# Optimization experiments

Hardware: AMD Instinct MI355X
Metric: run time of the kernel (lower is better)

Reference implementation:

```python
import jax, jax.numpy as jnp
import numpy as np

N_NODES = 50000
N_EDGES = 600000
CHANNELS = 128
HEADS = 8


def setup_inputs() -> dict:
    key = jax.random.key(0)
    k1, k2, k3 = jax.random.split(key, 3)
    x = jax.random.normal(k1, (N_NODES, CHANNELS), dtype=jnp.float32)
    edge_index = jax.random.randint(k2, (2, N_EDGES), 0, N_NODES, dtype=jnp.int32)
    att = jax.random.normal(k3, (HEADS, 2 * (CHANNELS // HEADS)), dtype=jnp.float32)
    return {"x": x, "edge_index": edge_index, "att": att}


def reference(x, edge_index, att):
    # x: [N, C], edge_index: [2, E], att: [H, 2*D] with D = C // H
    src, dst = edge_index[0], edge_index[1]
    n = x.shape[0]
    h = att.shape[0]
    d = att.shape[1] // 2

    x_src = x[src].reshape(-1, h, d)   # [E, H, D]
    x_dst = x[dst].reshape(-1, h, d)   # [E, H, D]

    # (cat([x_src, x_dst]) * att).sum(-1) == x_src @ att[:, :D] + x_dst @ att[:, D:]
    a_src, a_dst = att[:, :d], att[:, d:]
    alpha = jnp.einsum('ehd,hd->eh', x_src, a_src) + jnp.einsum('ehd,hd->eh', x_dst, a_dst)
    alpha = jnp.where(alpha >= 0, alpha, 0.2 * alpha)  # LeakyReLU(0.2)

    # segment softmax over dst; torch scatter_reduce amax includes the zero init,
    # so the per-node max is max(segment_max, 0)
    seg_max = jax.ops.segment_max(alpha, dst, num_segments=n)  # [N, H]
    seg_max = jnp.maximum(seg_max, 0.0)
    alpha = jnp.exp(alpha - seg_max[dst])
    seg_sum = jax.ops.segment_sum(alpha, dst, num_segments=n)  # [N, H]
    alpha = alpha / jnp.maximum(seg_sum[dst], 1e-10)

    # weighted scatter-add of source features
    weighted = x_src * alpha[..., None]                        # [E, H, D]
    out = jax.ops.segment_sum(weighted, dst, num_segments=n)   # [N, H, D]
    return out.reshape(n, -1)
```

## Files before the change

### kernel.cpp

```cpp
#include <hip/hip_runtime.h>

#define N_NODES  50000
#define N_EDGES  600000
#define CHANNELS 128
#define HEADS    8
#define HEAD_DIM 16
#define CAP      64

#define NBINS    256
#define CHUNK_E  1024
#define NCHUNK   ((N_EDGES + CHUNK_E - 1) / CHUNK_E)
#define SEGCAP   2816
#define NPB      200

#define LOGIT_VB ((N_NODES * (CHANNELS / 4)) / 256)
#define WPB      4

__global__ void hist_logit_kernel(const float* __restrict__ x,
                                  const float* __restrict__ att,
                                  const int*   __restrict__ dst,
                                  int*            __restrict__ hist,
                                  float*          __restrict__ ls8,
                                  float*          __restrict__ ld8,
                                  unsigned short* __restrict__ xb) {
    int b = blockIdx.x;
    int t = threadIdx.x;
    if (b < NCHUNK) {
        __shared__ int lh[NBINS];
        lh[t] = 0;
        __syncthreads();
        int base = b * CHUNK_E;
#pragma unroll
        for (int k = 0; k < 4; ++k) {
            int e = base + t + k * 256;
            if (e < N_EDGES) {
                unsigned bin = (unsigned)(dst[e] * NBINS) / N_NODES;
                atomicAdd(&lh[bin], 1);
            }
        }
        __syncthreads();
        hist[t * NCHUNK + b] = lh[t];
    } else {
        int gid = (b - NCHUNK) * 256 + t;
        int n  = gid >> 5;
        int c4 = gid & 31;
        int h  = c4 >> 2;
        int j4 = c4 & 3;

        float4 v = ((const float4*)x)[gid];

        unsigned int ux = __float_as_uint(v.x), uy = __float_as_uint(v.y);
        unsigned int uz = __float_as_uint(v.z), uw = __float_as_uint(v.w);
        ushort4 pk;
        pk.x = (unsigned short)((ux + 0x7FFFu + ((ux >> 16) & 1u)) >> 16);
        pk.y = (unsigned short)((uy + 0x7FFFu + ((uy >> 16) & 1u)) >> 16);
        pk.z = (unsigned short)((uz + 0x7FFFu + ((uz >> 16) & 1u)) >> 16);
        pk.w = (unsigned short)((uw + 0x7FFFu + ((uw >> 16) & 1u)) >> 16);
        ((ushort4*)xb)[gid] = pk;

        float4 as4 = ((const float4*)att)[h * 8 + j4];
        float4 ad4 = ((const float4*)att)[h * 8 + 4 + j4];
        float ts = v.x * as4.x + v.y * as4.y + v.z * as4.z + v.w * as4.w;
        float td = v.x * ad4.x + v.y * ad4.y + v.z * ad4.z + v.w * ad4.w;
        ts += __shfl_xor(ts, 1, 4); ts += __shfl_xor(ts, 2, 4);
        td += __shfl_xor(td, 1, 4); td += __shfl_xor(td, 2, 4);
        if (j4 == 0) {
            ls8[n * HEADS + h] = ts;
            ld8[n * HEADS + h] = td;
        }
    }
}

__global__ void scan_kernel(const int* __restrict__ hist,
                            int* __restrict__ offm,
                            int* __restrict__ bincnt) {
    __shared__ int lds[256];
    int bin = blockIdx.x;
    int t = threadIdx.x;
    int c0 = t, c1 = t + 256, c2 = t + 512;
    int v0 = hist[bin * NCHUNK + c0];
    int v1 = (c1 < NCHUNK) ? hist[bin * NCHUNK + c1] : 0;
    int v2 = (c2 < NCHUNK) ? hist[bin * NCHUNK + c2] : 0;
    int s = v0 + v1 + v2;
    lds[t] = s;
    __syncthreads();
    for (int off = 1; off < 256; off <<= 1) {
        int u = (t >= off) ? lds[t - off] : 0;
        __syncthreads();
        lds[t] += u;
        __syncthreads();
    }
    int base = lds[t] - s;
    offm[c0 * NBINS + bin] = base;
    if (c1 < NCHUNK) offm[c1 * NBINS + bin] = base + v0;
    if (c2 < NCHUNK) offm[c2 * NBINS + bin] = base + v0 + v1;
    if (t == 255) bincnt[bin] = lds[255];
}

__global__ void binscatter_kernel(const int* __restrict__ src,
                                  const int* __restrict__ dst,
                                  const int* __restrict__ offm,
                                  unsigned*  __restrict__ ebuf) {
    __shared__ int loff[NBINS];
    __shared__ int lcnt[NBINS];
    int b = blockIdx.x;
    int t = threadIdx.x;
    loff[t] = offm[b * NBINS + t];
    lcnt[t] = 0;
    __syncthreads();
    int base = b * CHUNK_E;
#pragma unroll
    for (int k = 0; k < 4; ++k) {
        int e = base + t + k * 256;
        if (e < N_EDGES) {
            int d = dst[e];
            int s = src[e];
            unsigned bin = (unsigned)(d * NBINS) / N_NODES;
            int r = atomicAdd(&lcnt[bin], 1) + loff[bin];
            if (r < SEGCAP)
                ebuf[(size_t)bin * SEGCAP + r] = (unsigned)s | ((unsigned)d << 16);
        }
    }
}

__global__ void bucket_kernel(const unsigned* __restrict__ ebuf,
                              const int*      __restrict__ bincnt,
                              int*            __restrict__ cursor,
                              unsigned short* __restrict__ bucket) {
    __shared__ unsigned short rows[NPB * CAP];
    __shared__ int lcnt[NPB];
    int b = blockIdx.x;
    int t = threadIdx.x;
    int n0 = (b * N_NODES + NBINS - 1) / NBINS;
    int n1 = ((b + 1) * N_NODES + NBINS - 1) / NBINS;
    int nn = n1 - n0;
    if (t < NPB) lcnt[t] = 0;
    __syncthreads();
    int cnt = min(bincnt[b], SEGCAP);
    for (int i = t; i < cnt; i += 256) {
        unsigned rec = ebuf[(size_t)b * SEGCAP + i];
        int s = (int)(rec & 0xFFFFu);
        int d = (int)(rec >> 16);
        int pos = atomicAdd(&lcnt[d - n0], 1);
        if (pos < CAP) rows[(d - n0) * CAP + pos] = (unsigned short)s;
    }
    __syncthreads();
    int nq = nn * (CAP * 2 / 16);
    uint4* gdst = (uint4*)(bucket + (size_t)n0 * CAP);
    const uint4* lsrc = (const uint4*)rows;
    for (int i = t; i < nq; i += 256) gdst[i] = lsrc[i];
    if (t < nn) cursor[n0 + t] = lcnt[t];
}

__global__ void fused_gat_kernel(const unsigned short* __restrict__ xb,
                                 const float* __restrict__ ls8,
                                 const float* __restrict__ ld8,
                                 const int*   __restrict__ cursor,
                                 const unsigned short* __restrict__ bucket,
                                 float*       __restrict__ out) {
    __shared__ float s_p[WPB * CAP * HEADS];

    int wave = threadIdx.x >> 6;
    int lane = threadIdx.x & 63;
    int n = blockIdx.x * WPB + wave;
    if (n >= N_NODES) return;
    int h = lane >> 3;
    int j = lane & 7;
    int r   = lane >> 5;
    int l32 = lane & 31;
    int h2  = l32 >> 2;

    int   cnt_raw = cursor[n];
    int   myidx   = (int)bucket[(size_t)n * CAP + lane];
    float ldst    = ld8[n * HEADS + h];
    int cnt = (cnt_raw > CAP) ? CAP : cnt_raw;

    float* sp = s_p + wave * (CAP * HEADS);

    float av[8];
    float mymax = -1e30f;
#pragma unroll
    for (int k = 0; k < 8; ++k) {
        int i = j + 8 * k;
        av[k] = -1e30f;
        if (i < cnt) {
            int   s  = __shfl(myidx, i);
            float lg = ls8[s * HEADS + h] + ldst;
            float a  = (lg >= 0.0f) ? lg : 0.2f * lg;
            av[k] = a;
            mymax = fmaxf(mymax, a);
        }
    }
#pragma unroll
    for (int o = 4; o >= 1; o >>= 1) mymax = fmaxf(mymax, __shfl_xor(mymax, o, 8));
    float m = fmaxf(mymax, 0.0f);

    float myl = 0.0f;
#pragma unroll
    for (int k = 0; k < 8; ++k) {
        int i = j + 8 * k;
        if (i < cnt) {
            float p = __expf(av[k] - m);
            sp[i * HEADS + h] = p;
            myl += p;
        }
    }
#pragma unroll
    for (int o = 4; o >= 1; o >>= 1) myl += __shfl_xor(myl, o, 8);

#define LP(k) ( ((const uint2*)(xb + (size_t)__shfl(myidx, ((2*(k)+r) < cnt) ? (2*(k)+r) : 0) * CHANNELS))[l32] )
    uint2 q[8];
#pragma unroll
    for (int k = 0; k < 8; ++k) q[k] = LP(k);

    float a0 = 0.f, a1 = 0.f, a2 = 0.f, a3 = 0.f;
    int npair = (cnt + 1) >> 1;
    int k = 0;
    for (; k + 4 <= npair; k += 4) {
#pragma unroll
        for (int u = 0; u < 4; ++u) {
            int e2 = 2 * (k + u) + r;
            float p = (e2 < cnt) ? sp[e2 * HEADS + h2] : 0.0f;
            uint2 qq = q[u];
            a0 += p * __uint_as_float(qq.x << 16);
            a1 += p * __uint_as_float(qq.x & 0xFFFF0000u);
            a2 += p * __uint_as_float(qq.y << 16);
            a3 += p * __uint_as_float(qq.y & 0xFFFF0000u);
        }
#pragma unroll
        for (int u = 0; u < 4; ++u) q[u] = q[u + 4];
#pragma unroll
        for (int u = 0; u < 4; ++u) q[u + 4] = LP(k + 8 + u);
    }
    for (; k < npair; ++k) {
        int e2 = 2 * k + r;
        float p = (e2 < cnt) ? sp[e2 * HEADS + h2] : 0.0f;
        uint2 qq = q[0];
        a0 += p * __uint_as_float(qq.x << 16);
        a1 += p * __uint_as_float(qq.x & 0xFFFF0000u);
        a2 += p * __uint_as_float(qq.y << 16);
        a3 += p * __uint_as_float(qq.y & 0xFFFF0000u);
#pragma unroll
        for (int u = 0; u < 7; ++u) q[u] = q[u + 1];
    }
#undef LP

    a0 += __shfl_xor(a0, 32);
    a1 += __shfl_xor(a1, 32);
    a2 += __shfl_xor(a2, 32);
    a3 += __shfl_xor(a3, 32);

    float denom = __shfl(myl, h2 * 8);
    float inv = 1.0f / fmaxf(denom, 1e-10f);

    if (lane < 32) {
        float4 o4 = make_float4(a0 * inv, a1 * inv, a2 * inv, a3 * inv);
        ((float4*)(out + (size_t)n * CHANNELS))[l32] = o4;
    }
}

extern "C" void kernel_launch(void* const* d_in, const int* in_sizes, int n_in,
                              void* d_out, int out_size, void* d_ws, size_t ws_size,
                              hipStream_t stream) {
    const float* x   = (const float*)d_in[0];
    const int*   ei  = (const int*)  d_in[1];
    const float* att = (const float*)d_in[2];
    const int* src = ei;
    const int* dst = ei + N_EDGES;
    float* out = (float*)d_out;

    int*            hist   = (int*)d_ws;
    int*            offm   = hist + (size_t)NBINS * NCHUNK;
    int*            bincnt = offm + (size_t)NCHUNK * NBINS;
    unsigned*       ebuf   = (unsigned*)(bincnt + NBINS);
    int*            cursor = (int*)(ebuf + (size_t)NBINS * SEGCAP);
    unsigned short* bucket = (unsigned short*)(cursor + N_NODES);
    float*          ls8    = (float*)(bucket + (size_t)N_NODES * CAP);
    float*          ld8    = ls8 + (size_t)N_NODES * HEADS;
    unsigned short* xb     = (unsigned short*)(ld8 + (size_t)N_NODES * HEADS);

    hist_logit_kernel<<<NCHUNK + LOGIT_VB, 256, 0, stream>>>(
        x, att, dst, hist, ls8, ld8, xb);
    scan_kernel<<<NBINS, 256, 0, stream>>>(hist, offm, bincnt);
    binscatter_kernel<<<NCHUNK, 256, 0, stream>>>(src, dst, offm, ebuf);
    bucket_kernel<<<NBINS, 256, 0, stream>>>(ebuf, bincnt, cursor, bucket);
    fused_gat_kernel<<<(N_NODES + WPB - 1) / WPB, 64 * WPB, 0, stream>>>(
        xb, ls8, ld8, cursor, bucket, out);
}
```

Baseline: 138.0 us.

## Fuse bucket build into GAT kernel with per-bin sub-blocks in shared memory

Merges the bucket kernel and the GAT aggregation kernel into one kernel. Each bin is split across 8 sub-blocks, and each sub-block builds its nodes' neighbor lists in LDS and then processes those nodes with waves looping over them. This removes the global bucket/cursor round trip and one kernel launch. In exchange, every sub-block rescans the whole bin's edge segment, which reads ebuf 8 times over. Only 2048 blocks are launched, each handling about 25 nodes, which lowers parallelism and can unbalance the load across blocks.

```diff
diff --git a/kernel.cpp b/kernel.cpp
--- a/kernel.cpp
+++ b/kernel.cpp
@@ -11,7 +11,9 @@
 #define CHUNK_E  1024
 #define NCHUNK   ((N_EDGES + CHUNK_E - 1) / CHUNK_E)
 #define SEGCAP   2816
-#define NPB      200
+
+#define SUBB     8
+#define NPB      25
 
 #define LOGIT_VB ((N_NODES * (CHANNELS / 4)) / 256)
 #define WPB      4
@@ -123,139 +125,137 @@
     }
 }
 
-__global__ void bucket_kernel(const unsigned* __restrict__ ebuf,
-                              const int*      __restrict__ bincnt,
-                              int*            __restrict__ cursor,
-                              unsigned short* __restrict__ bucket) {
+__global__ void binfused_kernel(const unsigned* __restrict__ ebuf,
+                                const int*      __restrict__ bincnt,
+                                const unsigned short* __restrict__ xb,
+                                const float* __restrict__ ls8,
+                                const float* __restrict__ ld8,
+                                float*       __restrict__ out) {
     __shared__ unsigned short rows[NPB * CAP];
-    __shared__ int lcnt[NPB];
-    int b = blockIdx.x;
-    int t = threadIdx.x;
-    int n0 = (b * N_NODES + NBINS - 1) / NBINS;
-    int n1 = ((b + 1) * N_NODES + NBINS - 1) / NBINS;
+    __shared__ int   lcnt[NPB];
+    __shared__ float s_p[WPB * CAP * HEADS];
+
+    int bin = blockIdx.x >> 3;
+    int sub = blockIdx.x & (SUBB - 1);
+    int t   = threadIdx.x;
+
+    int b0 = (bin * N_NODES + NBINS - 1) / NBINS;
+    int b1 = ((bin + 1) * N_NODES + NBINS - 1) / NBINS;
+    int bn = b1 - b0;
+    int n0 = b0 + (sub * bn) / SUBB;
+    int n1 = b0 + ((sub + 1) * bn) / SUBB;
     int nn = n1 - n0;
+
     if (t < NPB) lcnt[t] = 0;
     __syncthreads();
-    int cnt = min(bincnt[b], SEGCAP);
-    for (int i = t; i < cnt; i += 256) {
-        unsigned rec = ebuf[(size_t)b * SEGCAP + i];
-        int s = (int)(rec & 0xFFFFu);
+
+    int scnt = min(bincnt[bin], SEGCAP);
+    for (int i = t; i < scnt; i += 256) {
+        unsigned rec = ebuf[(size_t)bin * SEGCAP + i];
         int d = (int)(rec >> 16);
-        int pos = atomicAdd(&lcnt[d - n0], 1);
-        if (pos < CAP) rows[(d - n0) * CAP + pos] = (unsigned short)s;
-    }
-    __syncthreads();
-    int nq = nn * (CAP * 2 / 16);
-    uint4* gdst = (uint4*)(bucket + (size_t)n0 * CAP);
-    const uint4* lsrc = (const uint4*)rows;
-    for (int i = t; i < nq; i += 256) gdst[i] = lsrc[i];
-    if (t < nn) cursor[n0 + t] = lcnt[t];
-}
-
-__global__ void fused_gat_kernel(const unsigned short* __restrict__ xb,
-                                 const float* __restrict__ ls8,
-                                 const float* __restrict__ ld8,
-                                 const int*   __restrict__ cursor,
-                                 const unsigned short* __restrict__ bucket,
-                                 float*       __restrict__ out) {
-    __shared__ float s_p[WPB * CAP * HEADS];
-
-    int wave = threadIdx.x >> 6;
-    int lane = threadIdx.x & 63;
-    int n = blockIdx.x * WPB + wave;
-    if (n >= N_NODES) return;
+        if (d >= n0 && d < n1) {
+            int pos = atomicAdd(&lcnt[d - n0], 1);
+            if (pos < CAP) rows[(d - n0) * CAP + pos] = (unsigned short)(rec & 0xFFFFu);
+        }
+    }
+    __syncthreads();
+
+    int wave = t >> 6;
+    int lane = t & 63;
     int h = lane >> 3;
     int j = lane & 7;
     int r   = lane >> 5;
     int l32 = lane & 31;
     int h2  = l32 >> 2;
-
-    int   cnt_raw = cursor[n];
-    int   myidx   = (int)bucket[(size_t)n * CAP + lane];
-    float ldst    = ld8[n * HEADS + h];
-    int cnt = (cnt_raw > CAP) ? CAP : cnt_raw;
-
     float* sp = s_p + wave * (CAP * HEADS);
 
-    float av[8];
-    float mymax = -1e30f;
-#pragma unroll
-    for (int k = 0; k < 8; ++k) {
-        int i = j + 8 * k;
-        av[k] = -1e30f;
-        if (i < cnt) {
-            int   s  = __shfl(myidx, i);
-            float lg = ls8[s * HEADS + h] + ldst;
-            float a  = (lg >= 0.0f) ? lg : 0.2f * lg;
-            av[k] = a;
-            mymax = fmaxf(mymax, a);
-        }
-    }
-#pragma unroll
-    for (int o = 4; o >= 1; o >>= 1) mymax = fmaxf(mymax, __shfl_xor(mymax, o, 8));
-    float m = fmaxf(mymax, 0.0f);
-
-    float myl = 0.0f;
-#pragma unroll
-    for (int k = 0; k < 8; ++k) {
-        int i = j + 8 * k;
-        if (i < cnt) {
-            float p = __expf(av[k] - m);
-            sp[i * HEADS + h] = p;
-            myl += p;
-        }
-    }
-#pragma unroll
-    for (int o = 4; o >= 1; o >>= 1) myl += __shfl_xor(myl, o, 8);
+    for (int nl = wave; nl < nn; nl += WPB) {
+        int n = n0 + nl;
+        int cnt = lcnt[nl];
+        cnt = (cnt > CAP) ? CAP : cnt;
+        int   myidx = (int)rows[nl * CAP + lane];
+        float ldst  = ld8[n * HEADS + h];
+
+        float av[8];
+        float mymax = -1e30f;
+#pragma unroll
+        for (int k = 0; k < 8; ++k) {
+            int i = j + 8 * k;
+            av[k] = -1e30f;
+            if (i < cnt) {
+                int   s  = __shfl(myidx, i);
+                float lg = ls8[s * HEADS + h] + ldst;
+                float a  = (lg >= 0.0f) ? lg : 0.2f * lg;
+                av[k] = a;
+                mymax = fmaxf(mymax, a);
+            }
+        }
+#pragma unroll
+        for (int o = 4; o >= 1; o >>= 1) mymax = fmaxf(mymax, __shfl_xor(mymax, o, 8));
+        float m = fmaxf(mymax, 0.0f);
+
+        float myl = 0.0f;
+#pragma unroll
+        for (int k = 0; k < 8; ++k) {
+            int i = j + 8 * k;
+            if (i < cnt) {
+                float p = __expf(av[k] - m);
+                sp[i * HEADS + h] = p;
+                myl += p;
+            }
+        }
+#pragma unroll
+        for (int o = 4; o >= 1; o >>= 1) myl += __shfl_xor(myl, o, 8);
 
 #define LP(k) ( ((const uint2*)(xb + (size_t)__shfl(myidx, ((2*(k)+r) < cnt) ? (2*(k)+r) : 0) * CHANNELS))[l32] )
-    uint2 q[8];
-#pragma unroll
-    for (int k = 0; k < 8; ++k) q[k] = LP(k);
-
-    float a0 = 0.f, a1 = 0.f, a2 = 0.f, a3 = 0.f;
-    int npair = (cnt + 1) >> 1;
-    int k = 0;
-    for (; k + 4 <= npair; k += 4) {
-#pragma unroll
-        for (int u = 0; u < 4; ++u) {
-            int e2 = 2 * (k + u) + r;
+        uint2 q[8];
+#pragma unroll
+        for (int k = 0; k < 8; ++k) q[k] = LP(k);
+
+        float a0 = 0.f, a1 = 0.f, a2 = 0.f, a3 = 0.f;
+        int npair = (cnt + 1) >> 1;
+        int k = 0;
+        for (; k + 4 <= npair; k += 4) {
+#pragma unroll
+            for (int u = 0; u < 4; ++u) {
+                int e2 = 2 * (k + u) + r;
+                float p = (e2 < cnt) ? sp[e2 * HEADS + h2] : 0.0f;
+                uint2 qq = q[u];
+                a0 += p * __uint_as_float(qq.x << 16);
+                a1 += p * __uint_as_float(qq.x & 0xFFFF0000u);
+                a2 += p * __uint_as_float(qq.y << 16);
+                a3 += p * __uint_as_float(qq.y & 0xFFFF0000u);
+            }
+#pragma unroll
+            for (int u = 0; u < 4; ++u) q[u] = q[u + 4];
+#pragma unroll
+            for (int u = 0; u < 4; ++u) q[u + 4] = LP(k + 8 + u);
+        }
+        for (; k < npair; ++k) {
+            int e2 = 2 * k + r;
             float p = (e2 < cnt) ? sp[e2 * HEADS + h2] : 0.0f;
-            uint2 qq = q[u];
+            uint2 qq = q[0];
             a0 += p * __uint_as_float(qq.x << 16);
             a1 += p * __uint_as_float(qq.x & 0xFFFF0000u);
             a2 += p * __uint_as_float(qq.y << 16);
             a3 += p * __uint_as_float(qq.y & 0xFFFF0000u);
-        }
-#pragma unroll
-        for (int u = 0; u < 4; ++u) q[u] = q[u + 4];
-#pragma unroll
-        for (int u = 0; u < 4; ++u) q[u + 4] = LP(k + 8 + u);
-    }
-    for (; k < npair; ++k) {
-        int e2 = 2 * k + r;
-        float p = (e2 < cnt) ? sp[e2 * HEADS + h2] : 0.0f;
-        uint2 qq = q[0];
-        a0 += p * __uint_as_float(qq.x << 16);
-        a1 += p * __uint_as_float(qq.x & 0xFFFF0000u);
-        a2 += p * __uint_as_float(qq.y << 16);
-        a3 += p * __uint_as_float(qq.y & 0xFFFF0000u);
-#pragma unroll
-        for (int u = 0; u < 7; ++u) q[u] = q[u + 1];
-    }
+#pragma unroll
+            for (int u = 0; u < 7; ++u) q[u] = q[u + 1];
+        }
 #undef LP
 
-    a0 += __shfl_xor(a0, 32);
-    a1 += __shfl_xor(a1, 32);
-    a2 += __shfl_xor(a2, 32);
-    a3 += __shfl_xor(a3, 32);
-
-    float denom = __shfl(myl, h2 * 8);
-    float inv = 1.0f / fmaxf(denom, 1e-10f);
-
-    if (lane < 32) {
-        float4 o4 = make_float4(a0 * inv, a1 * inv, a2 * inv, a3 * inv);
-        ((float4*)(out + (size_t)n * CHANNELS))[l32] = o4;
+        a0 += __shfl_xor(a0, 32);
+        a1 += __shfl_xor(a1, 32);
+        a2 += __shfl_xor(a2, 32);
+        a3 += __shfl_xor(a3, 32);
+
+        float denom = __shfl(myl, h2 * 8);
+        float inv = 1.0f / fmaxf(denom, 1e-10f);
+
+        if (lane < 32) {
+            float4 o4 = make_float4(a0 * inv, a1 * inv, a2 * inv, a3 * inv);
+            ((float4*)(out + (size_t)n * CHANNELS))[l32] = o4;
+        }
     }
 }
 
@@ -273,9 +273,7 @@
     int*            offm   = hist + (size_t)NBINS * NCHUNK;
     int*            bincnt = offm + (size_t)NCHUNK * NBINS;
     unsigned*       ebuf   = (unsigned*)(bincnt + NBINS);
-    int*            cursor = (int*)(ebuf + (size_t)NBINS * SEGCAP);
-    unsigned short* bucket = (unsigned short*)(cursor + N_NODES);
-    float*          ls8    = (float*)(bucket + (size_t)N_NODES * CAP);
+    float*          ls8    = (float*)(ebuf + (size_t)NBINS * SEGCAP);
     float*          ld8    = ls8 + (size_t)N_NODES * HEADS;
     unsigned short* xb     = (unsigned short*)(ld8 + (size_t)N_NODES * HEADS);
 
@@ -283,7 +281,6 @@
         x, att, dst, hist, ls8, ld8, xb);
     scan_kernel<<<NBINS, 256, 0, stream>>>(hist, offm, bincnt);
     binscatter_kernel<<<NCHUNK, 256, 0, stream>>>(src, dst, offm, ebuf);
-    bucket_kernel<<<NBINS, 256, 0, stream>>>(ebuf, bincnt, cursor, bucket);
-    fused_gat_kernel<<<(N_NODES + WPB - 1) / WPB, 64 * WPB, 0, stream>>>(
-        xb, ls8, ld8, cursor, bucket, out);
-}
+    binfused_kernel<<<NBINS * SUBB, 64 * WPB, 0, stream>>>(
+        ebuf, bincnt, xb, ls8, ld8, out);
+}
```

Result: slower. 146.0 us (+5.8%).
